# Kernel optimization log

Hardware: AMD Instinct MI355X
Metric: run time of the kernel (lower is better)

Reference implementation:

```python
import jax, jax.numpy as jnp
import numpy as np

T_STEPS = 200       # num_diffusion_steps
NUM_CLASSES = 21
PRECISION = 1e-4
EPS = 1e-10


def _alpha_cumprod(num_steps=T_STEPS, precision=PRECISION):
    steps = jnp.arange(num_steps + 1, dtype=jnp.float32) / num_steps
    ac = jnp.cos((steps + precision) / (1.0 + precision) * jnp.pi / 2.0) ** 2
    ac = ac / ac[0]
    betas = jnp.clip(1.0 - ac[1:] / ac[:-1], 0.0, 0.999)
    alphas = 1.0 - betas
    return jnp.cumprod(alphas)


def setup_inputs() -> dict:
    key = jax.random.key(0)
    k1, k2 = jax.random.split(key)
    B, S, C = 64, 4096, NUM_CLASSES
    x_0 = jax.random.uniform(k1, (B, S, C), dtype=jnp.float32)
    t = jax.random.randint(k2, (B,), 0, T_STEPS)
    return {"x_0": x_0, "t": t}


def reference(x_0, t):
    # q_sample(x_0, t, return_logits=True)
    B, S, C = x_0.shape
    alpha_t = _alpha_cumprod()[t]                     # [B]
    target = 1.0 / C                                   # uniform target distribution
    eye = jnp.eye(C, dtype=x_0.dtype)
    # transition matrix is constant over seq positions: [B, C, C]
    q_small = alpha_t[:, None, None] * eye + (1.0 - alpha_t)[:, None, None] * target
    log_q = jnp.log(q_small + EPS)                     # [B, C, C]
    # x_0^T @ log(q_t): contract over source class axis
    logits = jnp.einsum('bsc,bcd->bsd', x_0, log_q)    # [B, S, C]
    # module returns the full per-position transition tensor as well
    q_t = jnp.broadcast_to(q_small[:, None], (B, S, C, C))
    return logits, q_t
```

## Files before the change

kernel.cpp:

```cpp
#include <hip/hip_runtime.h>
#include <hip/hip_bf16.h>
#include <math.h>

#define NB 64
#define NS 4096
#define NC 21
#define NCC 441
#define TSTEPS 200


__global__ __launch_bounds__(512) void schedule_kernel(const int* __restrict__ t,
                                                       float* __restrict__ ws) {
    int b = blockIdx.x;
    __shared__ float s_alpha;
    if (threadIdx.x == 0) {
        int tb = t[b];
        const float HPI = 1.5707963267948966f;
        const float P = 1e-4f;
        float cum = 1.0f;
        float alpha = 1.0f;
        for (int i = 0; i < TSTEPS; ++i) {
            float s0 = ((float)i / (float)TSTEPS + P) / (1.0f + P) * HPI;
            float s1 = ((float)(i + 1) / (float)TSTEPS + P) / (1.0f + P) * HPI;
            float c0 = cosf(s0);
            float c1 = cosf(s1);
            float beta = 1.0f - (c1 * c1) / (c0 * c0);
            beta = fminf(fmaxf(beta, 0.0f), 0.999f);
            cum *= (1.0f - beta);
            if (i == tb) { alpha = cum; break; }
        }
        s_alpha = alpha;
        ws[b] = alpha;
    }
    __syncthreads();
    float a = s_alpha;
    float off = (1.0f - a) / (float)NC;
    float* lq = ws + NB + (size_t)b * NCC;
    for (int k = threadIdx.x; k < NCC; k += blockDim.x) {
        float q = off + ((k % 22) == 0 ? a : 0.0f);
        lq[k] = logf(q + 1e-10f);
    }
}

__global__ __launch_bounds__(256) void logits_kernel(const float* __restrict__ x0,
                                                     const float* __restrict__ ws,
                                                     float* __restrict__ out) {
    __shared__ float s_logq[NCC];
    __shared__ float s_x[256 * NC];
    const int blocksPerBatch = NS / 256;
    int b  = blockIdx.x / blocksPerBatch;
    int p0 = (blockIdx.x % blocksPerBatch) * 256;

    const float* lq = ws + NB + (size_t)b * NCC;
    for (int k = threadIdx.x; k < NCC; k += 256) s_logq[k] = lq[k];

    size_t base = ((size_t)b * NS + p0) * NC;
    for (int i = threadIdx.x; i < 256 * NC; i += 256) s_x[i] = x0[base + i];
    __syncthreads();

    float x[NC];
#pragma unroll
    for (int c = 0; c < NC; ++c) x[c] = s_x[threadIdx.x * NC + c];

    float acc[NC];
#pragma unroll
    for (int d = 0; d < NC; ++d) acc[d] = 0.0f;
#pragma unroll
    for (int c = 0; c < NC; ++c) {
        float xc = x[c];
#pragma unroll
        for (int d = 0; d < NC; ++d)
            acc[d] = fmaf(xc, s_logq[c * NC + d], acc[d]);
    }
    __syncthreads();
#pragma unroll
    for (int d = 0; d < NC; ++d) s_x[threadIdx.x * NC + d] = acc[d];
    __syncthreads();
    for (int i = threadIdx.x; i < 256 * NC; i += 256) out[base + i] = s_x[i];
}

__global__ __launch_bounds__(256) void qt_kernel(const float* __restrict__ ws,
                                                 float* __restrict__ qt) {
    int b = blockIdx.y;
    float a = ws[b];
    float off = (1.0f - a) / (float)NC;
    const unsigned N4 = NS * NCC / 4;
    float4* dst = (float4*)(qt + (size_t)b * NS * NCC);
    unsigned stride = gridDim.x * blockDim.x;
    for (unsigned i4 = blockIdx.x * blockDim.x + threadIdx.x; i4 < N4; i4 += stride) {
        unsigned f  = i4 * 4u;
        unsigned k0 = f % 441u;
        unsigned r0 = k0 % 22u;
        float4 v;
        float* vp = (float*)&v;
#pragma unroll
        for (int m = 0; m < 4; ++m) {
            unsigned km = k0 + (unsigned)m;
            unsigned rm = r0 + (unsigned)m;
            if (km >= 441u) rm = km - 441u;
            bool diag = (rm == 0u) || (rm == 22u);
            vp[m] = off + (diag ? a : 0.0f);
        }
        dst[i4] = v;
    }
}

extern "C" void kernel_launch(void* const* d_in, const int* in_sizes, int n_in,
                              void* d_out, int out_size, void* d_ws, size_t ws_size,
                              hipStream_t stream) {
    const float* x0 = (const float*)d_in[0];
    const int*   t  = (const int*)d_in[1];
    float* out    = (float*)d_out;
    float* logits = out;
    float* qt     = out + (size_t)NB * NS * NC;
    float* ws     = (float*)d_ws;

    schedule_kernel<<<NB, 512, 0, stream>>>(t, ws);
    logits_kernel<<<(NB * NS) / 256, 256, 0, stream>>>(x0, ws, logits);
    qt_kernel<<<dim3(128, NB), 256, 0, stream>>>(ws, qt);
}
```

Measured before the change: 557.8 us.

## Fuse logits and transition-matrix writes into one kernel with closed-form logits

```diff
diff --git a/kernel.cpp b/kernel.cpp
--- a/kernel.cpp
+++ b/kernel.cpp
@@ -9,99 +9,99 @@
 #define TSTEPS 200
 
 
-__global__ __launch_bounds__(512) void schedule_kernel(const int* __restrict__ t,
-                                                       float* __restrict__ ws) {
-    int b = blockIdx.x;
-    __shared__ float s_alpha;
-    if (threadIdx.x == 0) {
-        int tb = t[b];
-        const float HPI = 1.5707963267948966f;
-        const float P = 1e-4f;
-        float cum = 1.0f;
-        float alpha = 1.0f;
-        for (int i = 0; i < TSTEPS; ++i) {
-            float s0 = ((float)i / (float)TSTEPS + P) / (1.0f + P) * HPI;
-            float s1 = ((float)(i + 1) / (float)TSTEPS + P) / (1.0f + P) * HPI;
-            float c0 = cosf(s0);
-            float c1 = cosf(s1);
-            float beta = 1.0f - (c1 * c1) / (c0 * c0);
-            beta = fminf(fmaxf(beta, 0.0f), 0.999f);
-            cum *= (1.0f - beta);
-            if (i == tb) { alpha = cum; break; }
-        }
-        s_alpha = alpha;
-        ws[b] = alpha;
+__global__ __launch_bounds__(64) void schedule_kernel(const int* __restrict__ t,
+                                                      float4* __restrict__ ws) {
+    int b = threadIdx.x;
+    int tb = t[b];
+    const float HPI = 1.5707963267948966f;
+    const float P = 1e-4f;
+    float cum = 1.0f;
+    float alpha = 1.0f;
+    float c0 = __cosf(P / (1.0f + P) * HPI);
+    for (int i = 0; i < TSTEPS; ++i) {
+        float s1 = ((float)(i + 1) / (float)TSTEPS + P) / (1.0f + P) * HPI;
+        float c1 = __cosf(s1);
+        float beta = 1.0f - (c1 * c1) / (c0 * c0);
+        beta = fminf(fmaxf(beta, 0.0f), 0.999f);
+        cum *= (1.0f - beta);
+        if (i == tb) alpha = cum;
+        c0 = c1;
     }
-    __syncthreads();
-    float a = s_alpha;
-    float off = (1.0f - a) / (float)NC;
-    float* lq = ws + NB + (size_t)b * NCC;
-    for (int k = threadIdx.x; k < NCC; k += blockDim.x) {
-        float q = off + ((k % 22) == 0 ? a : 0.0f);
-        lq[k] = logf(q + 1e-10f);
-    }
+    float qo = (1.0f - alpha) / (float)NC;
+    float qd = qo + alpha;
+    float Loff  = logf(qo + 1e-10f);
+    float Ldiag = logf(qd + 1e-10f);
+    ws[b] = make_float4(qo, qd, Loff, Ldiag - Loff);
 }
 
-__global__ __launch_bounds__(256) void logits_kernel(const float* __restrict__ x0,
-                                                     const float* __restrict__ ws,
-                                                     float* __restrict__ out) {
-    __shared__ float s_logq[NCC];
-    __shared__ float s_x[256 * NC];
-    const int blocksPerBatch = NS / 256;
-    int b  = blockIdx.x / blocksPerBatch;
-    int p0 = (blockIdx.x % blocksPerBatch) * 256;
+__global__ __launch_bounds__(256) void fused_kernel(const float* __restrict__ x0,
+                                                    const float4* __restrict__ ws,
+                                                    float* __restrict__ logits,
+                                                    float* __restrict__ qt) {
+    __shared__ float4 s4[1344];
+    const int tid = threadIdx.x;
+    const int id = blockIdx.x;
+    const int div17 = id / 17;
 
-    const float* lq = ws + NB + (size_t)b * NCC;
-    for (int k = threadIdx.x; k < NCC; k += 256) s_logq[k] = lq[k];
+    if (id % 17 != 0) {
+        const int blk = id - 1 - div17;
+        const int b = blk >> 8;
+        const float4 w = ws[b];
+        const float qo = w.x, qd = w.y;
 
-    size_t base = ((size_t)b * NS + p0) * NC;
-    for (int i = threadIdx.x; i < 256 * NC; i += 256) s_x[i] = x0[base + i];
-    __syncthreads();
+        for (int k = tid; k < NCC; k += 256) {
+            int p0 = 4 * k;
+            if (p0 >= 882) p0 -= 882;
+            if (p0 >= 441) p0 -= 441;
+            float4 v;
+            float* vp = (float*)&v;
+#pragma unroll
+            for (int m = 0; m < 4; ++m) {
+                int pm = p0 + m;
+                if (pm >= 441) pm -= 441;
+                vp[m] = (pm % 22 == 0) ? qd : qo;
+            }
+            s4[k] = v;
+        }
+        __syncthreads();
 
-    float x[NC];
+        float4* dst = (float4*)qt + (size_t)blk * 1764;
+        for (int i = tid; i < 1764; i += 256) {
+            int m = i;
+            if (m >= 882) m -= 882;
+            if (m >= 441) m -= 441;
+            dst[i] = s4[m];
+        }
+    } else {
+        const int blk = div17;
+        const int b = blk >> 4;
+        const float4 w = ws[b];
+        const float Loff = w.z, Ldelta = w.w;
+
+        const float4* g = (const float4*)x0 + (size_t)blk * 1344;
 #pragma unroll
-    for (int c = 0; c < NC; ++c) x[c] = s_x[threadIdx.x * NC + c];
+        for (int k = 0; k < 6; ++k) {
+            int idx = tid + k * 256;
+            if (idx < 1344) s4[idx] = g[idx];
+        }
+        __syncthreads();
 
-    float acc[NC];
+        float* sf = (float*)s4;
+        float x[NC];
+        float S = 0.0f;
 #pragma unroll
-    for (int d = 0; d < NC; ++d) acc[d] = 0.0f;
+        for (int c = 0; c < NC; ++c) { x[c] = sf[tid * NC + c]; S += x[c]; }
+        float base = Loff * S;
 #pragma unroll
-    for (int c = 0; c < NC; ++c) {
-        float xc = x[c];
+        for (int d = 0; d < NC; ++d) sf[tid * NC + d] = fmaf(Ldelta, x[d], base);
+        __syncthreads();
+
+        float4* o = (float4*)logits + (size_t)blk * 1344;
 #pragma unroll
-        for (int d = 0; d < NC; ++d)
-            acc[d] = fmaf(xc, s_logq[c * NC + d], acc[d]);
-    }
-    __syncthreads();
-#pragma unroll
-    for (int d = 0; d < NC; ++d) s_x[threadIdx.x * NC + d] = acc[d];
-    __syncthreads();
-    for (int i = threadIdx.x; i < 256 * NC; i += 256) out[base + i] = s_x[i];
-}
-
-__global__ __launch_bounds__(256) void qt_kernel(const float* __restrict__ ws,
-                                                 float* __restrict__ qt) {
-    int b = blockIdx.y;
-    float a = ws[b];
-    float off = (1.0f - a) / (float)NC;
-    const unsigned N4 = NS * NCC / 4;
-    float4* dst = (float4*)(qt + (size_t)b * NS * NCC);
-    unsigned stride = gridDim.x * blockDim.x;
-    for (unsigned i4 = blockIdx.x * blockDim.x + threadIdx.x; i4 < N4; i4 += stride) {
-        unsigned f  = i4 * 4u;
-        unsigned k0 = f % 441u;
-        unsigned r0 = k0 % 22u;
-        float4 v;
-        float* vp = (float*)&v;
-#pragma unroll
-        for (int m = 0; m < 4; ++m) {
-            unsigned km = k0 + (unsigned)m;
-            unsigned rm = r0 + (unsigned)m;
-            if (km >= 441u) rm = km - 441u;
-            bool diag = (rm == 0u) || (rm == 22u);
-            vp[m] = off + (diag ? a : 0.0f);
+        for (int k = 0; k < 6; ++k) {
+            int idx = tid + k * 256;
+            if (idx < 1344) o[idx] = s4[idx];
         }
-        dst[i4] = v;
     }
 }
 
@@ -113,9 +113,8 @@
     float* out    = (float*)d_out;
     float* logits = out;
     float* qt     = out + (size_t)NB * NS * NC;
-    float* ws     = (float*)d_ws;
+    float4* ws    = (float4*)d_ws;
 
-    schedule_kernel<<<NB, 512, 0, stream>>>(t, ws);
-    logits_kernel<<<(NB * NS) / 256, 256, 0, stream>>>(x0, ws, logits);
-    qt_kernel<<<dim3(128, NB), 256, 0, stream>>>(ws, qt);
+    schedule_kernel<<<1, 64, 0, stream>>>(t, ws);
+    fused_kernel<<<17408, 256, 0, stream>>>(x0, ws, logits, qt);
 }
```

After: 522.4 us. 6.3% less time.
